# Optimization experiments

Measured on AMD Instinct MI355X. Metric: run time of the kernel, lower is better.

## Reference

```python
import jax, jax.numpy as jnp
import numpy as np

BASE_LR = 0.1
LN_EPS = 1e-5
D_IN = 1024
D_OUT = 1024
BATCH = 16384


def setup_inputs() -> dict:
    key = jax.random.key(0)
    ks = jax.random.split(key, 5)
    x = jax.random.normal(ks[0], (BATCH, D_IN), dtype=jnp.float32)
    plasticity = jax.random.uniform(ks[1], (BATCH,), dtype=jnp.float32)
    alpha = jax.random.uniform(ks[2], (1,), dtype=jnp.float32)
    # Parameters / buffers (orthogonal / kaiming init approximated with scaled normals)
    W_slow = jax.random.normal(ks[3], (D_OUT, D_IN), dtype=jnp.float32) * (1.4 / np.sqrt(D_IN))
    bound = 1.0 / np.sqrt(D_IN)  # kaiming_uniform with a=sqrt(5) on [d_out, d_in]
    W_fast = jax.random.uniform(ks[4], (D_OUT, D_IN), dtype=jnp.float32, minval=-bound, maxval=bound)
    gamma = jnp.ones((D_OUT,), dtype=jnp.float32)
    beta = jnp.zeros((D_OUT,), dtype=jnp.float32)
    return {"x": x, "plasticity": plasticity, "alpha": alpha,
            "W_slow": W_slow, "W_fast": W_fast, "gamma": gamma, "beta": beta}


def reference(x, plasticity, alpha, W_slow, W_fast, gamma, beta):
    # Dual linear reads: [B, d_in] @ [d_in, d_out]
    slow = x @ W_slow.T           # [B, d_out]
    fast = x @ W_fast.T           # [B, d_out]

    # Hebbian fast-weight update (training branch, no-grad in original)
    batch = x.shape[0]
    hebb = (fast.T @ x) / batch                         # [d_out, d_in]
    forget = jnp.mean(fast ** 2, axis=0)[:, None] * W_fast  # [d_out, d_in]
    eff_lr = jnp.mean(plasticity) * BASE_LR             # scalar, kept on-device
    W_fast_new = W_fast + jnp.tanh(hebb - forget) * eff_lr

    # Combine + LayerNorm over last dim
    combined = slow + fast * alpha                      # alpha broadcast scalar
    mu = jnp.mean(combined, axis=-1, keepdims=True)
    var = jnp.mean((combined - mu) ** 2, axis=-1, keepdims=True)
    out = (combined - mu) * jax.lax.rsqrt(var + LN_EPS) * gamma + beta
    return (out, slow, W_fast_new)
```

## Files before the change

### kernel.cpp

```cpp
#include <hip/hip_runtime.h>
#include <cstdint>
#include <cstddef>

#define B_SZ 16384
#define DIN  1024
#define DOUT 1024
#define SPLITK 8

typedef short bf16x8 __attribute__((ext_vector_type(8)));
typedef float f32x4  __attribute__((ext_vector_type(4)));

static __device__ __forceinline__ short f2bf(float f) {
    union { float f; unsigned u; } v; v.f = f;
    unsigned r = v.u + 0x7fffu + ((v.u >> 16) & 1u);
    return (short)(r >> 16);
}
static __device__ __forceinline__ float bf2f(short s) {
    union { unsigned u; float f; } v; v.u = ((unsigned)(unsigned short)s) << 16;
    return v.f;
}
static __device__ __forceinline__ void gload_lds16(const short* g, short* l) {
    __builtin_amdgcn_global_load_lds(
        (const __attribute__((address_space(1))) void*)g,
        (__attribute__((address_space(3))) void*)l, 16, 0, 0);
}

__global__ __launch_bounds__(256) void convert_f32_bf16(const float* __restrict__ in,
                                                        short* __restrict__ out, int n4) {
    int i = blockIdx.x * 256 + threadIdx.x;
    if (i < n4) {
        float4 v = ((const float4*)in)[i];
        short4 o;
        o.x = f2bf(v.x); o.y = f2bf(v.y); o.z = f2bf(v.z); o.w = f2bf(v.w);
        ((short4*)out)[i] = o;
    }
}

__global__ __launch_bounds__(256) void x_convert(const float* __restrict__ x,
                                                 short* __restrict__ xb,
                                                 short* __restrict__ xT) {
    __shared__ short t[64 * 72];
    const int b0 = blockIdx.x * 64;
    const int d0 = blockIdx.y * 64;
    const int tid = threadIdx.x;
    const int r = tid >> 2;
    const int c = (tid & 3) * 16;
    short loc[16];
    #pragma unroll
    for (int i = 0; i < 4; ++i) {
        float4 v = *(const float4*)&x[(size_t)(b0 + r) * DIN + d0 + c + i * 4];
        loc[i * 4 + 0] = f2bf(v.x); loc[i * 4 + 1] = f2bf(v.y);
        loc[i * 4 + 2] = f2bf(v.z); loc[i * 4 + 3] = f2bf(v.w);
    }
    *(bf16x8*)&xb[(size_t)(b0 + r) * DIN + d0 + c]     = *(bf16x8*)&loc[0];
    *(bf16x8*)&xb[(size_t)(b0 + r) * DIN + d0 + c + 8] = *(bf16x8*)&loc[8];
    #pragma unroll
    for (int i = 0; i < 16; ++i) t[(c + i) * 72 + r] = loc[i];
    __syncthreads();
    const int d = tid >> 2, bs = (tid & 3) * 16;
    *(bf16x8*)&xT[(size_t)(d0 + d) * B_SZ + b0 + bs]     = *(bf16x8*)&t[d * 72 + bs];
    *(bf16x8*)&xT[(size_t)(d0 + d) * B_SZ + b0 + bs + 8] = *(bf16x8*)&t[d * 72 + bs + 8];
}

__global__ __launch_bounds__(256) void fast_trans(const float* __restrict__ fast,
                                                  short* __restrict__ fastT) {
    __shared__ short t[64 * 72];
    const int b0 = blockIdx.x * 64;
    const int d0 = blockIdx.y * 64;
    const int tid = threadIdx.x;
    const int r = tid >> 2;
    const int c = (tid & 3) * 16;
    short loc[16];
    #pragma unroll
    for (int i = 0; i < 4; ++i) {
        float4 v = *(const float4*)&fast[(size_t)(b0 + r) * DOUT + d0 + c + i * 4];
        loc[i * 4 + 0] = f2bf(v.x); loc[i * 4 + 1] = f2bf(v.y);
        loc[i * 4 + 2] = f2bf(v.z); loc[i * 4 + 3] = f2bf(v.w);
    }
    #pragma unroll
    for (int i = 0; i < 16; ++i) t[(c + i) * 72 + r] = loc[i];
    __syncthreads();
    const int d = tid >> 2, bs = (tid & 3) * 16;
    *(bf16x8*)&fastT[(size_t)(d0 + d) * B_SZ + b0 + bs]     = *(bf16x8*)&t[d * 72 + bs];
    *(bf16x8*)&fastT[(size_t)(d0 + d) * B_SZ + b0 + bs + 8] = *(bf16x8*)&t[d * 72 + bs + 8];
}

__global__ __launch_bounds__(256) void init_kernel(const float* __restrict__ plast,
                                                   float* __restrict__ eff_lr) {
    int tid = threadIdx.x;
    float s = 0.f;
    for (int i = tid; i < B_SZ; i += 256) s += plast[i];
    __shared__ float red[256];
    red[tid] = s; __syncthreads();
    for (int off = 128; off > 0; off >>= 1) {
        if (tid < off) red[tid] += red[tid + off];
        __syncthreads();
    }
    if (tid == 0) eff_lr[0] = (red[0] / (float)B_SZ) * 0.1f;
}

__global__ __launch_bounds__(256) void dual_gemm(
    const short* __restrict__ Xb,
    const short* __restrict__ Wc,
    float* __restrict__ slow_out,
    float* __restrict__ fast_out)
{
    __shared__ short lA[128 * 32];
    __shared__ short lB[128 * 32];
    const int tid = threadIdx.x;
    const int lane = tid & 63;
    const int wave = tid >> 6;
    const int wm = wave & 1, wn = wave >> 1;
    const int quad = lane >> 4, l16 = lane & 15;
    const int m0 = blockIdx.x * 128;
    const int n0 = blockIdx.y * 128;
    const int lrow = lane >> 2;
    const int lcol = (lane & 3) * 8;

    f32x4 acc[4][4] = {};

    const short* gA0 = &Xb[(size_t)(m0 + wave * 32 + lrow) * DIN + lcol];
    const short* gA1 = gA0 + (size_t)16 * DIN;
    const short* gB0 = &Wc[(size_t)(n0 + wave * 32 + lrow) * DIN + lcol];
    const short* gB1 = gB0 + (size_t)16 * DIN;
    short* sA0 = &lA[(wave * 32) * 32];
    short* sA1 = &lA[(wave * 32 + 16) * 32];
    short* sB0 = &lB[(wave * 32) * 32];
    short* sB1 = &lB[(wave * 32 + 16) * 32];

    for (int k0 = 0; k0 < DIN; k0 += 32) {
        gload_lds16(gA0 + k0, sA0);
        gload_lds16(gA1 + k0, sA1);
        gload_lds16(gB0 + k0, sB0);
        gload_lds16(gB1 + k0, sB1);
        __syncthreads();
        bf16x8 af[4], bfr[4];
        #pragma unroll
        for (int t = 0; t < 4; ++t) {
            af[t]  = *(const bf16x8*)&lA[(wm * 64 + t * 16 + l16) * 32 + quad * 8];
            bfr[t] = *(const bf16x8*)&lB[(wn * 64 + t * 16 + l16) * 32 + quad * 8];
        }
        #pragma unroll
        for (int tm = 0; tm < 4; ++tm)
            #pragma unroll
            for (int tn = 0; tn < 4; ++tn)
                acc[tm][tn] = __builtin_amdgcn_mfma_f32_16x16x32_bf16(af[tm], bfr[tn], acc[tm][tn], 0, 0, 0);
        __syncthreads();
    }
    float* dst = (n0 < 1024) ? slow_out : fast_out;
    const int cb = (n0 < 1024) ? n0 : n0 - 1024;
    #pragma unroll
    for (int tm = 0; tm < 4; ++tm) {
        int r0 = m0 + wm * 64 + tm * 16 + quad * 4;
        #pragma unroll
        for (int tn = 0; tn < 4; ++tn) {
            int cc = cb + wn * 64 + tn * 16 + l16;
            #pragma unroll
            for (int r = 0; r < 4; ++r)
                dst[(size_t)(r0 + r) * 1024 + cc] = acc[tm][tn][r];
        }
    }
}

__global__ __launch_bounds__(256) void hebb_gemm(
    const short* __restrict__ fastT,
    const short* __restrict__ xT,
    short* __restrict__ hebb_part)
{
    __shared__ short lA[128 * 32];
    __shared__ short lB[128 * 32];
    const int tid = threadIdx.x;
    const int lane = tid & 63;
    const int wave = tid >> 6;
    const int wm = wave & 1, wn = wave >> 1;
    const int quad = lane >> 4, l16 = lane & 15;
    const int m0 = blockIdx.x * 128;
    const int n0 = blockIdx.y * 128;
    const int kb = blockIdx.z * (B_SZ / SPLITK);
    const int lrow = lane >> 2;
    const int lcol = (lane & 3) * 8;

    f32x4 acc[4][4] = {};

    const short* gA0 = &fastT[(size_t)(m0 + wave * 32 + lrow) * B_SZ + kb + lcol];
    const short* gA1 = gA0 + (size_t)16 * B_SZ;
    const short* gB0 = &xT[(size_t)(n0 + wave * 32 + lrow) * B_SZ + kb + lcol];
    const short* gB1 = gB0 + (size_t)16 * B_SZ;
    short* sA0 = &lA[(wave * 32) * 32];
    short* sA1 = &lA[(wave * 32 + 16) * 32];
    short* sB0 = &lB[(wave * 32) * 32];
    short* sB1 = &lB[(wave * 32 + 16) * 32];

    for (int k0 = 0; k0 < B_SZ / SPLITK; k0 += 32) {
        gload_lds16(gA0 + k0, sA0);
        gload_lds16(gA1 + k0, sA1);
        gload_lds16(gB0 + k0, sB0);
        gload_lds16(gB1 + k0, sB1);
        __syncthreads();
        bf16x8 af[4], bfr[4];
        #pragma unroll
        for (int t = 0; t < 4; ++t) {
            af[t]  = *(const bf16x8*)&lA[(wm * 64 + t * 16 + l16) * 32 + quad * 8];
            bfr[t] = *(const bf16x8*)&lB[(wn * 64 + t * 16 + l16) * 32 + quad * 8];
        }
        #pragma unroll
        for (int tm = 0; tm < 4; ++tm)
            #pragma unroll
            for (int tn = 0; tn < 4; ++tn)
                acc[tm][tn] = __builtin_amdgcn_mfma_f32_16x16x32_bf16(af[tm], bfr[tn], acc[tm][tn], 0, 0, 0);
        __syncthreads();
    }
    short* dst = hebb_part + (size_t)blockIdx.z * DOUT * DIN;
    #pragma unroll
    for (int tm = 0; tm < 4; ++tm) {
        int r0 = m0 + wm * 64 + tm * 16 + quad * 4;
        #pragma unroll
        for (int tn = 0; tn < 4; ++tn) {
            int cc = n0 + wn * 64 + tn * 16 + l16;
            #pragma unroll
            for (int r = 0; r < 4; ++r)
                dst[(size_t)(r0 + r) * DIN + cc] = f2bf(acc[tm][tn][r]);
        }
    }
}

__global__ __launch_bounds__(256) void colsumsq_kernel(const short* __restrict__ fastT,
                                                       float* __restrict__ sums) {
    const int m = blockIdx.x;
    const int tid = threadIdx.x;
    const short* row = &fastT[(size_t)m * B_SZ];
    float s = 0.f;
    for (int i = tid * 8; i < B_SZ; i += 256 * 8) {
        bf16x8 v = *(const bf16x8*)&row[i];
        #pragma unroll
        for (int j = 0; j < 8; ++j) { float f = bf2f(v[j]); s += f * f; }
    }
    __shared__ float red[256];
    red[tid] = s; __syncthreads();
    for (int off = 128; off > 0; off >>= 1) {
        if (tid < off) red[tid] += red[tid + off];
        __syncthreads();
    }
    if (tid == 0) sums[m] = red[0];
}

__global__ __launch_bounds__(256) void wfast_update(
    const float* __restrict__ Wf, const short* __restrict__ hebb_part,
    const float* __restrict__ colsumsq, const float* __restrict__ eff_lr,
    float* __restrict__ Wf_new)
{
    const int i0 = (blockIdx.x * 256 + threadIdx.x) * 8;
    const int m = i0 >> 10;
    const float lr = eff_lr[0];
    const float fgm = colsumsq[m] * (1.0f / (float)B_SZ);
    float h[8] = {0.f, 0.f, 0.f, 0.f, 0.f, 0.f, 0.f, 0.f};
    #pragma unroll
    for (int z = 0; z < SPLITK; ++z) {
        bf16x8 v = *(const bf16x8*)&hebb_part[(size_t)z * DOUT * DIN + i0];
        #pragma unroll
        for (int j = 0; j < 8; ++j) h[j] += bf2f(v[j]);
    }
    float4 w0 = *(const float4*)&Wf[i0];
    float4 w1 = *(const float4*)&Wf[i0 + 4];
    float w[8] = {w0.x, w0.y, w0.z, w0.w, w1.x, w1.y, w1.z, w1.w};
    float o[8];
    #pragma unroll
    for (int j = 0; j < 8; ++j)
        o[j] = w[j] + tanhf(h[j] * (1.0f / (float)B_SZ) - fgm * w[j]) * lr;
    *(float4*)&Wf_new[i0]     = make_float4(o[0], o[1], o[2], o[3]);
    *(float4*)&Wf_new[i0 + 4] = make_float4(o[4], o[5], o[6], o[7]);
}

__global__ __launch_bounds__(256) void ln_kernel(
    const float* __restrict__ slow, float* __restrict__ io,
    const float* __restrict__ gamma, const float* __restrict__ beta,
    const float* __restrict__ alpha)
{
    const int row = blockIdx.x;
    const int tid = threadIdx.x;
    const float a = alpha[0];
    const size_t base = (size_t)row * DOUT;
    float c[4];
    float s = 0.f, ss = 0.f;
    #pragma unroll
    for (int i = 0; i < 4; ++i) {
        int col = tid + i * 256;
        float v = slow[base + col] + a * io[base + col];
        c[i] = v; s += v; ss += v * v;
    }
    #pragma unroll
    for (int off = 32; off > 0; off >>= 1) {
        s  += __shfl_down(s, off);
        ss += __shfl_down(ss, off);
    }
    __shared__ float rs[4], rss[4];
    int wave = tid >> 6;
    if ((tid & 63) == 0) { rs[wave] = s; rss[wave] = ss; }
    __syncthreads();
    float S  = rs[0] + rs[1] + rs[2] + rs[3];
    float SS = rss[0] + rss[1] + rss[2] + rss[3];
    float mu = S * (1.0f / DOUT);
    float var = SS * (1.0f / DOUT) - mu * mu;
    float inv = rsqrtf(var + 1e-5f);
    #pragma unroll
    for (int i = 0; i < 4; ++i) {
        int col = tid + i * 256;
        io[base + col] = (c[i] - mu) * inv * gamma[col] + beta[col];
    }
}

extern "C" void kernel_launch(void* const* d_in, const int* in_sizes, int n_in,
                              void* d_out, int out_size, void* d_ws, size_t ws_size,
                              hipStream_t stream)
{
    const float* x     = (const float*)d_in[0];
    const float* plast = (const float*)d_in[1];
    const float* alpha = (const float*)d_in[2];
    const float* Wslow = (const float*)d_in[3];
    const float* Wfast = (const float*)d_in[4];
    const float* gamma = (const float*)d_in[5];
    const float* beta  = (const float*)d_in[6];

    float* out   = (float*)d_out;
    float* slow  = out + (size_t)B_SZ * DOUT;
    float* wfnew = slow + (size_t)B_SZ * DOUT;

    char* ws = (char*)d_ws;
    short* xb    = (short*)ws;
    short* fastT = xb;
    short* xT    = (short*)(ws + (size_t)B_SZ * DIN * 2);
    short* wcat  = xT + (size_t)DIN * B_SZ;
    short* hebb  = wcat + (size_t)2048 * DIN;
    float* csq   = (float*)(hebb + (size_t)SPLITK * DOUT * DIN);
    float* efflr = csq + DOUT;

    x_convert<<<dim3(B_SZ / 64, DIN / 64), 256, 0, stream>>>(x, xb, xT);
    convert_f32_bf16<<<(DOUT * DIN / 4 + 255) / 256, 256, 0, stream>>>(Wslow, wcat, DOUT * DIN / 4);
    convert_f32_bf16<<<(DOUT * DIN / 4 + 255) / 256, 256, 0, stream>>>(Wfast, wcat + (size_t)DOUT * DIN, DOUT * DIN / 4);
    init_kernel<<<1, 256, 0, stream>>>(plast, efflr);
    dual_gemm<<<dim3(B_SZ / 128, 2048 / 128), 256, 0, stream>>>(xb, wcat, slow, out);
    fast_trans<<<dim3(B_SZ / 64, DOUT / 64), 256, 0, stream>>>(out, fastT);
    colsumsq_kernel<<<DOUT, 256, 0, stream>>>(fastT, csq);
    hebb_gemm<<<dim3(DOUT / 128, DIN / 128, SPLITK), 256, 0, stream>>>(fastT, xT, hebb);
    wfast_update<<<(DOUT * DIN) / (256 * 8), 256, 0, stream>>>(Wfast, hebb, csq, efflr, wfnew);
    ln_kernel<<<B_SZ, 256, 0, stream>>>(slow, out, gamma, beta, alpha);
}
```

Baseline: 437.3 us.

## Fuse fast transpose into dual GEMM epilogue, raise hebb split-K, vectorize LayerNorm

When the workspace is large enough, the dual GEMM epilogue also writes a transposed bf16 copy of the fast output. This removes the separate fast_trans kernel and its re-read of the fp32 fast matrix. The hebb GEMM split-K count goes from 8 to 16 for more parallelism, which doubles the partial buffers that wfast_update must reduce. LayerNorm now uses float4 loads and stores. The transposed epilogue writes are 8-byte scattered stores with a stride of B_SZ, so they may be poorly coalesced.

```diff
diff --git a/kernel.cpp b/kernel.cpp
--- a/kernel.cpp
+++ b/kernel.cpp
@@ -5,7 +5,6 @@
 #define B_SZ 16384
 #define DIN  1024
 #define DOUT 1024
-#define SPLITK 8
 
 typedef short bf16x8 __attribute__((ext_vector_type(8)));
 typedef float f32x4  __attribute__((ext_vector_type(4)));
@@ -103,7 +102,8 @@
     const short* __restrict__ Xb,
     const short* __restrict__ Wc,
     float* __restrict__ slow_out,
-    float* __restrict__ fast_out)
+    float* __restrict__ fast_out,
+    short* __restrict__ fastT)
 {
     __shared__ short lA[128 * 32];
     __shared__ short lB[128 * 32];
@@ -147,17 +147,35 @@
                 acc[tm][tn] = __builtin_amdgcn_mfma_f32_16x16x32_bf16(af[tm], bfr[tn], acc[tm][tn], 0, 0, 0);
         __syncthreads();
     }
-    float* dst = (n0 < 1024) ? slow_out : fast_out;
-    const int cb = (n0 < 1024) ? n0 : n0 - 1024;
-    #pragma unroll
-    for (int tm = 0; tm < 4; ++tm) {
-        int r0 = m0 + wm * 64 + tm * 16 + quad * 4;
-        #pragma unroll
-        for (int tn = 0; tn < 4; ++tn) {
-            int cc = cb + wn * 64 + tn * 16 + l16;
-            #pragma unroll
-            for (int r = 0; r < 4; ++r)
-                dst[(size_t)(r0 + r) * 1024 + cc] = acc[tm][tn][r];
+    if (n0 < 1024) {
+        #pragma unroll
+        for (int tm = 0; tm < 4; ++tm) {
+            int r0 = m0 + wm * 64 + tm * 16 + quad * 4;
+            #pragma unroll
+            for (int tn = 0; tn < 4; ++tn) {
+                int cc = n0 + wn * 64 + tn * 16 + l16;
+                #pragma unroll
+                for (int r = 0; r < 4; ++r)
+                    slow_out[(size_t)(r0 + r) * 1024 + cc] = acc[tm][tn][r];
+            }
+        }
+    } else {
+        #pragma unroll
+        for (int tm = 0; tm < 4; ++tm) {
+            int r0 = m0 + wm * 64 + tm * 16 + quad * 4;
+            #pragma unroll
+            for (int tn = 0; tn < 4; ++tn) {
+                int cc = (n0 - 1024) + wn * 64 + tn * 16 + l16;
+                #pragma unroll
+                for (int r = 0; r < 4; ++r)
+                    fast_out[(size_t)(r0 + r) * 1024 + cc] = acc[tm][tn][r];
+                if (fastT) {
+                    short4 p;
+                    p.x = f2bf(acc[tm][tn][0]); p.y = f2bf(acc[tm][tn][1]);
+                    p.z = f2bf(acc[tm][tn][2]); p.w = f2bf(acc[tm][tn][3]);
+                    *(short4*)&fastT[(size_t)cc * B_SZ + r0] = p;
+                }
+            }
         }
     }
 }
@@ -165,7 +183,8 @@
 __global__ __launch_bounds__(256) void hebb_gemm(
     const short* __restrict__ fastT,
     const short* __restrict__ xT,
-    short* __restrict__ hebb_part)
+    short* __restrict__ hebb_part,
+    int kchunk)
 {
     __shared__ short lA[128 * 32];
     __shared__ short lB[128 * 32];
@@ -176,7 +195,7 @@
     const int quad = lane >> 4, l16 = lane & 15;
     const int m0 = blockIdx.x * 128;
     const int n0 = blockIdx.y * 128;
-    const int kb = blockIdx.z * (B_SZ / SPLITK);
+    const int kb = blockIdx.z * kchunk;
     const int lrow = lane >> 2;
     const int lcol = (lane & 3) * 8;
 
@@ -191,7 +210,7 @@
     short* sB0 = &lB[(wave * 32) * 32];
     short* sB1 = &lB[(wave * 32 + 16) * 32];
 
-    for (int k0 = 0; k0 < B_SZ / SPLITK; k0 += 32) {
+    for (int k0 = 0; k0 < kchunk; k0 += 32) {
         gload_lds16(gA0 + k0, sA0);
         gload_lds16(gA1 + k0, sA1);
         gload_lds16(gB0 + k0, sB0);
@@ -247,15 +266,14 @@
 __global__ __launch_bounds__(256) void wfast_update(
     const float* __restrict__ Wf, const short* __restrict__ hebb_part,
     const float* __restrict__ colsumsq, const float* __restrict__ eff_lr,
-    float* __restrict__ Wf_new)
+    float* __restrict__ Wf_new, int nsplit)
 {
     const int i0 = (blockIdx.x * 256 + threadIdx.x) * 8;
     const int m = i0 >> 10;
     const float lr = eff_lr[0];
     const float fgm = colsumsq[m] * (1.0f / (float)B_SZ);
     float h[8] = {0.f, 0.f, 0.f, 0.f, 0.f, 0.f, 0.f, 0.f};
-    #pragma unroll
-    for (int z = 0; z < SPLITK; ++z) {
+    for (int z = 0; z < nsplit; ++z) {
         bf16x8 v = *(const bf16x8*)&hebb_part[(size_t)z * DOUT * DIN + i0];
         #pragma unroll
         for (int j = 0; j < 8; ++j) h[j] += bf2f(v[j]);
@@ -280,14 +298,13 @@
     const int tid = threadIdx.x;
     const float a = alpha[0];
     const size_t base = (size_t)row * DOUT;
-    float c[4];
+    const int col = tid * 4;
+    float4 sv = *(const float4*)&slow[base + col];
+    float4 fv = *(const float4*)&io[base + col];
+    float c[4] = {sv.x + a * fv.x, sv.y + a * fv.y, sv.z + a * fv.z, sv.w + a * fv.w};
     float s = 0.f, ss = 0.f;
     #pragma unroll
-    for (int i = 0; i < 4; ++i) {
-        int col = tid + i * 256;
-        float v = slow[base + col] + a * io[base + col];
-        c[i] = v; s += v; ss += v * v;
-    }
+    for (int i = 0; i < 4; ++i) { s += c[i]; ss += c[i] * c[i]; }
     #pragma unroll
     for (int off = 32; off > 0; off >>= 1) {
         s  += __shfl_down(s, off);
@@ -302,11 +319,14 @@
     float mu = S * (1.0f / DOUT);
     float var = SS * (1.0f / DOUT) - mu * mu;
     float inv = rsqrtf(var + 1e-5f);
-    #pragma unroll
-    for (int i = 0; i < 4; ++i) {
-        int col = tid + i * 256;
-        io[base + col] = (c[i] - mu) * inv * gamma[col] + beta[col];
-    }
+    float4 gv = *(const float4*)&gamma[col];
+    float4 bv = *(const float4*)&beta[col];
+    float4 ov;
+    ov.x = (c[0] - mu) * inv * gv.x + bv.x;
+    ov.y = (c[1] - mu) * inv * gv.y + bv.y;
+    ov.z = (c[2] - mu) * inv * gv.z + bv.z;
+    ov.w = (c[3] - mu) * inv * gv.w + bv.w;
+    *(float4*)&io[base + col] = ov;
 }
 
 extern "C" void kernel_launch(void* const* d_in, const int* in_sizes, int n_in,
@@ -325,23 +345,37 @@
     float* slow  = out + (size_t)B_SZ * DOUT;
     float* wfnew = slow + (size_t)B_SZ * DOUT;
 
+    const size_t MB = 1ull << 20;
     char* ws = (char*)d_ws;
-    short* xb    = (short*)ws;
-    short* fastT = xb;
-    short* xT    = (short*)(ws + (size_t)B_SZ * DIN * 2);
-    short* wcat  = xT + (size_t)DIN * B_SZ;
-    short* hebb  = wcat + (size_t)2048 * DIN;
-    float* csq   = (float*)(hebb + (size_t)SPLITK * DOUT * DIN);
+    short* xb   = (short*)ws;
+    short* xT   = (short*)(ws + 32 * MB);
+    short* wcat = (short*)(ws + 64 * MB);
+
+    const bool fused = ws_size >= 101 * MB;
+    short* fastT; short* hebb; float* csq; int nsplit;
+    if (fused) {
+        fastT = (short*)(ws + 68 * MB);
+        hebb  = xb;
+        csq   = (float*)(ws + 100 * MB);
+        nsplit = 16;
+    } else {
+        fastT = xb;
+        hebb  = (short*)(ws + 68 * MB);
+        csq   = (float*)(ws + 84 * MB);
+        nsplit = 8;
+    }
     float* efflr = csq + DOUT;
 
     x_convert<<<dim3(B_SZ / 64, DIN / 64), 256, 0, stream>>>(x, xb, xT);
     convert_f32_bf16<<<(DOUT * DIN / 4 + 255) / 256, 256, 0, stream>>>(Wslow, wcat, DOUT * DIN / 4);
     convert_f32_bf16<<<(DOUT * DIN / 4 + 255) / 256, 256, 0, stream>>>(Wfast, wcat + (size_t)DOUT * DIN, DOUT * DIN / 4);
     init_kernel<<<1, 256, 0, stream>>>(plast, efflr);
-    dual_gemm<<<dim3(B_SZ / 128, 2048 / 128), 256, 0, stream>>>(xb, wcat, slow, out);
-    fast_trans<<<dim3(B_SZ / 64, DOUT / 64), 256, 0, stream>>>(out, fastT);
+    dual_gemm<<<dim3(B_SZ / 128, 2048 / 128), 256, 0, stream>>>(xb, wcat, slow, out,
+                                                                fused ? fastT : (short*)nullptr);
+    if (!fused)
+        fast_trans<<<dim3(B_SZ / 64, DOUT / 64), 256, 0, stream>>>(out, fastT);
     colsumsq_kernel<<<DOUT, 256, 0, stream>>>(fastT, csq);
-    hebb_gemm<<<dim3(DOUT / 128, DIN / 128, SPLITK), 256, 0, stream>>>(fastT, xT, hebb);
-    wfast_update<<<(DOUT * DIN) / (256 * 8), 256, 0, stream>>>(Wfast, hebb, csq, efflr, wfnew);
+    hebb_gemm<<<dim3(DOUT / 128, DIN / 128, nsplit), 256, 0, stream>>>(fastT, xT, hebb, B_SZ / nsplit);
+    wfast_update<<<(DOUT * DIN) / (256 * 8), 256, 0, stream>>>(Wfast, hebb, csq, efflr, wfnew, nsplit);
     ln_kernel<<<B_SZ, 256, 0, stream>>>(slow, out, gamma, beta, alpha);
 }
```

After: 451.2 us. +3.2%, slower.
